# Performance work log

Measured on AMD Instinct MI355X. Metric: run time of the kernel, lower is better.

Reference implementation:

```python
import jax, jax.numpy as jnp
import numpy as np

N_NODES = 100000
N_EDGES = 1600000
HIDDEN = 64
IN_DIM = 3
OUT_DIM = 2
N_MP = 3


def setup_inputs() -> dict:
    key = jax.random.key(0)
    ks = jax.random.split(key, 16)
    x = jax.random.normal(ks[0], (N_NODES, IN_DIM), dtype=jnp.float32)
    edge_index = jax.random.randint(ks[1], (2, N_EDGES), 0, N_NODES, dtype=jnp.int64)

    def lin(k, fan_in, fan_out):
        s = 1.0 / np.sqrt(fan_in)
        return jax.random.uniform(k, (fan_out, fan_in), jnp.float32, -s, s)

    inp = {
        'x': x,
        'edge_index': edge_index,
        'preW': lin(ks[2], IN_DIM, HIDDEN),
        'preb': jnp.zeros((HIDDEN,), jnp.float32),
        'postW': lin(ks[3], HIDDEN, OUT_DIM),
        'postb': jnp.zeros((OUT_DIM,), jnp.float32),
    }
    for i in range(N_MP):
        inp[f'relW{i}'] = lin(ks[4 + 3 * i], HIDDEN, HIDDEN)
        inp[f'relb{i}'] = jnp.zeros((HIDDEN,), jnp.float32)
        inp[f'rootW{i}'] = lin(ks[5 + 3 * i], HIDDEN, HIDDEN)
    return inp


def _graph_conv(h, src, dst, relW, relb, rootW):
    # PyG GraphConv: out_i = W_rel @ (sum_{j in N(i)} h_j) + b_rel + W_root @ h_i
    agg = jax.ops.segment_sum(h[src], dst, num_segments=N_NODES)  # [N, H] scatter-add
    return agg @ relW.T + relb + h @ rootW.T


def reference(x, edge_index, preW, preb, postW, postb,
              relW0, relb0, rootW0, relW1, relb1, rootW1, relW2, relb2, rootW2):
    src, dst = edge_index[0], edge_index[1]
    # pre-MP dense
    h = jax.nn.relu(x @ preW.T + preb)
    # message passing layers (GraphConv, aggr='add'), relu after each
    for relW, relb, rootW in ((relW0, relb0, rootW0),
                              (relW1, relb1, rootW1),
                              (relW2, relb2, rootW2)):
        h = jax.nn.relu(_graph_conv(h, src, dst, relW, relb, rootW))
    # post-MP dense (activation applied to final layer too, as in source)
    out = jax.nn.relu(h @ postW.T + postb)
    return out
```

## Files before the change

### kernel.cpp

```cpp
#include <hip/hip_runtime.h>
#include <hip/hip_fp16.h>

#define N_NODES 100000
#define N_EDGES 1600000
#define HID 64

#define BSH 8
#define NBKT ((N_NODES + 255) / 256)
#define CAP 6144
#define TILE 4096
#define NCHUNK ((N_EDGES + TILE - 1) / TILE)

#define HSC 0.015625f
#define HSCI 64.0f

typedef _Float16 f16x8 __attribute__((ext_vector_type(8)));
typedef float f32x4 __attribute__((ext_vector_type(4)));

__global__ void __launch_bounds__(512) fused0_kernel(
    const int* __restrict__ src, const int* __restrict__ dst,
    int* __restrict__ bcur, unsigned int* __restrict__ tmp,
    const float* __restrict__ x, const float* __restrict__ preW,
    const float* __restrict__ preb, const float* __restrict__ relW,
    const float* __restrict__ relb, const float* __restrict__ rootW,
    __half* __restrict__ m, __half* __restrict__ aout) {
    extern __shared__ __align__(16) char smem[];
    int tid = threadIdx.x;
    if (blockIdx.x < NCHUNK) {
        unsigned long long* ed = (unsigned long long*)smem;
        int* cnt = (int*)(smem + 32768);
        int* cnt2 = (int*)(smem + 34368);
        int* scnx = (int*)(smem + 35968);
        int* gbase = (int*)(smem + 37568);
        int* s = (int*)(smem + 39168);
        int bstart = blockIdx.x * TILE;
        int tcnt = N_EDGES - bstart;
        if (tcnt > TILE) tcnt = TILE;
        if (tcnt < 0) tcnt = 0;
        for (int b = tid; b < NBKT; b += 512) { cnt[b] = 0; cnt2[b] = 0; }
        __syncthreads();
        for (int i = tid; i < tcnt; i += 512) atomicAdd(&cnt[dst[bstart + i] >> BSH], 1);
        __syncthreads();
        s[tid] = (tid < NBKT) ? cnt[tid] : 0;
        __syncthreads();
        for (int off = 1; off < 512; off <<= 1) {
            int add = (tid >= off) ? s[tid - off] : 0;
            __syncthreads();
            s[tid] += add;
            __syncthreads();
        }
        if (tid < NBKT) {
            scnx[tid] = s[tid] - cnt[tid];
            gbase[tid] = tid * CAP + atomicAdd(&bcur[tid], cnt[tid]);
        }
        __syncthreads();
        for (int i = tid; i < tcnt; i += 512) {
            int e = bstart + i;
            int d = dst[e], sc = src[e];
            int b = d >> BSH;
            int pos = scnx[b] + atomicAdd(&cnt2[b], 1);
            ed[pos] = ((unsigned long long)(unsigned)d << 32) | (unsigned)sc;
        }
        __syncthreads();
        for (int i = tid; i < tcnt; i += 512) {
            unsigned long long v = ed[i];
            int d = (int)(v >> 32);
            unsigned sc = (unsigned)v;
            int b = d >> BSH;
            int idx = gbase[b] + (i - scnx[b]);
            if (idx < (b + 1) * CAP)
                tmp[idx] = ((unsigned)(d & 255) << 17) | sc;
        }
    } else {
        __half* hs = (__half*)smem;
        __half* ws = (__half*)(smem + 16384);
        float* xs = (float*)(smem + 32768);
        float* pw = (float*)(smem + 34304);
        float* pbs = (float*)(smem + 35072);
        int g = blockIdx.x - NCHUNK;
        int i0 = g * 128;
#pragma unroll
        for (int it = 0; it < 2; it++) {
            int t = it * 512 + tid;
            int row = t >> 3, c = t & 7;
            const float* wsrc = (row < 64) ? &relW[row * 64 + c * 8]
                                           : &rootW[(row - 64) * 64 + c * 8];
            float4 w0 = *(const float4*)wsrc;
            float4 w1 = *(const float4*)(wsrc + 4);
            uint4 pk;
            __half2* hp = (__half2*)&pk;
            hp[0] = __floats2half2_rn(w0.x, w0.y);
            hp[1] = __floats2half2_rn(w0.z, w0.w);
            hp[2] = __floats2half2_rn(w1.x, w1.y);
            hp[3] = __floats2half2_rn(w1.z, w1.w);
            *(uint4*)&ws[row * 64 + ((c ^ (row & 7)) << 3)] = pk;
        }
        if (tid < 192) pw[tid] = preW[tid];
        if (tid < 64) pbs[tid] = preb[tid];
        if (tid < 384) {
            int gi = i0 * 3 + tid;
            xs[tid] = (gi < N_NODES * 3) ? x[gi] : 0.f;
        }
        __syncthreads();
#pragma unroll
        for (int it = 0; it < 2; it++) {
            int t = it * 512 + tid;
            int row = t >> 3, c = t & 7;
            float v[8];
#pragma unroll
            for (int u = 0; u < 8; u++) {
                int col = c * 8 + u;
                float sv = pbs[col];
                sv = fmaf(xs[row * 3 + 0], pw[col * 3 + 0], sv);
                sv = fmaf(xs[row * 3 + 1], pw[col * 3 + 1], sv);
                sv = fmaf(xs[row * 3 + 2], pw[col * 3 + 2], sv);
                v[u] = fmaxf(sv, 0.f);
            }
            uint4 pk;
            __half2* hp = (__half2*)&pk;
            hp[0] = __floats2half2_rn(v[0], v[1]);
            hp[1] = __floats2half2_rn(v[2], v[3]);
            hp[2] = __floats2half2_rn(v[4], v[5]);
            hp[3] = __floats2half2_rn(v[6], v[7]);
            *(uint4*)&hs[row * 64 + ((c ^ (row & 7)) << 3)] = pk;
        }
        __syncthreads();
        int lane = tid & 63;
        int w = tid >> 6;
        int wm = w >> 1, wn = w & 1;
        int r = lane & 15, q = lane >> 4;
        f32x4 acc[2][4];
#pragma unroll
        for (int mt = 0; mt < 2; mt++)
#pragma unroll
            for (int nt = 0; nt < 4; nt++) acc[mt][nt] = (f32x4){0.f, 0.f, 0.f, 0.f};
#pragma unroll
        for (int ks = 0; ks < 2; ks++) {
            f16x8 af[2], bf[4];
#pragma unroll
            for (int mt = 0; mt < 2; mt++) {
                int row = wm * 32 + mt * 16 + r;
                int cc = (ks * 4 + q) ^ (row & 7);
                af[mt] = *(const f16x8*)&hs[row * 64 + (cc << 3)];
            }
#pragma unroll
            for (int nt = 0; nt < 4; nt++) {
                int row = wn * 64 + nt * 16 + r;
                int cc = (ks * 4 + q) ^ (row & 7);
                bf[nt] = *(const f16x8*)&ws[row * 64 + (cc << 3)];
            }
#pragma unroll
            for (int mt = 0; mt < 2; mt++)
#pragma unroll
                for (int nt = 0; nt < 4; nt++)
                    acc[mt][nt] = __builtin_amdgcn_mfma_f32_16x16x32_f16(af[mt], bf[nt],
                                                                         acc[mt][nt], 0, 0, 0);
        }
        if (wn == 0) {
#pragma unroll
            for (int mt = 0; mt < 2; mt++) {
                int nb = i0 + wm * 32 + mt * 16 + q * 4;
#pragma unroll
                for (int reg = 0; reg < 4; reg++) {
                    int node = nb + reg;
                    if (node >= N_NODES) continue;
#pragma unroll
                    for (int nt = 0; nt < 4; nt++)
                        m[(long)node * 64 + nt * 16 + r] = __float2half(acc[mt][nt][reg]);
                }
            }
        } else {
            float rb[4];
#pragma unroll
            for (int nt = 0; nt < 4; nt++) rb[nt] = relb[nt * 16 + r] * HSC;
#pragma unroll
            for (int mt = 0; mt < 2; mt++) {
                int nb = i0 + wm * 32 + mt * 16 + q * 4;
#pragma unroll
                for (int reg = 0; reg < 4; reg++) {
                    int node = nb + reg;
                    if (node >= N_NODES) continue;
#pragma unroll
                    for (int nt = 0; nt < 4; nt++)
                        aout[(long)node * 64 + nt * 16 + r] =
                            __float2half(fmaf(acc[mt][nt][reg], HSC, rb[nt]));
                }
            }
        }
    }
}

__global__ void __launch_bounds__(256) passb_kernel(const unsigned int* __restrict__ tmp,
                                                    const int* __restrict__ bcur,
                                                    int* __restrict__ rowp,
                                                    int* __restrict__ ssrc) {
    __shared__ int red[256];
    __shared__ int cnt[256], s[256], cur[256];
    int tid = threadIdx.x;
    int b = blockIdx.x;
    int acc = 0;
    for (int i = tid; i < b; i += 256) {
        int c = bcur[i];
        if (c > CAP) c = CAP;
        acc += c;
    }
    red[tid] = acc;
    __syncthreads();
    for (int off = 128; off >= 1; off >>= 1) {
        if (tid < off) red[tid] += red[tid + off];
        __syncthreads();
    }
    int lo = red[0];
    int ne = bcur[b];
    if (ne > CAP) ne = CAP;
    if (b == NBKT - 1 && tid == 0) rowp[N_NODES] = lo + ne;
    int lo_t = b * CAP;
    cnt[tid] = 0;
    __syncthreads();
    for (int i = tid; i < ne; i += 256) atomicAdd(&cnt[tmp[lo_t + i] >> 17], 1);
    __syncthreads();
    int v = cnt[tid];
    s[tid] = v;
    __syncthreads();
    for (int off = 1; off < 256; off <<= 1) {
        int a = (tid >= off) ? s[tid - off] : 0;
        __syncthreads();
        s[tid] += a;
        __syncthreads();
    }
    int excl = lo + s[tid] - v;
    int node = (b << BSH) + tid;
    if (node < N_NODES) rowp[node] = excl;
    cur[tid] = excl;
    __syncthreads();
    for (int i = tid; i < ne; i += 256) {
        unsigned u = tmp[lo_t + i];
        int pos = atomicAdd(&cur[u >> 17], 1);
        ssrc[pos] = (int)(u & 0x1FFFF);
    }
}

__global__ void __launch_bounds__(256) gemmt_kernel(const __half* __restrict__ h,
                                                    const float* __restrict__ relW,
                                                    const float* __restrict__ relb,
                                                    const float* __restrict__ rootW,
                                                    __half* __restrict__ m,
                                                    __half* __restrict__ aout) {
    __shared__ __align__(16) __half hs[128 * 64];
    __shared__ __align__(16) __half ws[128 * 64];
    int tid = threadIdx.x;
    int i0 = blockIdx.x * 128;
#pragma unroll
    for (int it = 0; it < 4; it++) {
        int t = it * 256 + tid;
        int row = t >> 3, c = t & 7;
        const float* wsrc = (row < 64) ? &relW[row * 64 + c * 8]
                                       : &rootW[(row - 64) * 64 + c * 8];
        float4 w0 = *(const float4*)wsrc;
        float4 w1 = *(const float4*)(wsrc + 4);
        uint4 pk;
        __half2* hp = (__half2*)&pk;
        hp[0] = __floats2half2_rn(w0.x, w0.y);
        hp[1] = __floats2half2_rn(w0.z, w0.w);
        hp[2] = __floats2half2_rn(w1.x, w1.y);
        hp[3] = __floats2half2_rn(w1.z, w1.w);
        *(uint4*)&ws[row * 64 + ((c ^ (row & 7)) << 3)] = pk;
    }
#pragma unroll
    for (int it = 0; it < 4; it++) {
        int t = it * 256 + tid;
        int row = t >> 3, c = t & 7;
        uint4 hv = {0u, 0u, 0u, 0u};
        if (i0 + row < N_NODES) hv = *(const uint4*)(h + (long)(i0 + row) * 64 + c * 8);
        *(uint4*)&hs[row * 64 + ((c ^ (row & 7)) << 3)] = hv;
    }
    __syncthreads();

    int lane = tid & 63;
    int w = tid >> 6;
    int wm = w >> 1, wn = w & 1;
    int r = lane & 15, q = lane >> 4;
    f32x4 acc[4][4];
#pragma unroll
    for (int mt = 0; mt < 4; mt++)
#pragma unroll
        for (int nt = 0; nt < 4; nt++) acc[mt][nt] = (f32x4){0.f, 0.f, 0.f, 0.f};
#pragma unroll
    for (int ks = 0; ks < 2; ks++) {
        f16x8 af[4], bf[4];
#pragma unroll
        for (int mt = 0; mt < 4; mt++) {
            int row = wm * 64 + mt * 16 + r;
            int cc = (ks * 4 + q) ^ (row & 7);
            af[mt] = *(const f16x8*)&hs[row * 64 + (cc << 3)];
        }
#pragma unroll
        for (int nt = 0; nt < 4; nt++) {
            int row = wn * 64 + nt * 16 + r;
            int cc = (ks * 4 + q) ^ (row & 7);
            bf[nt] = *(const f16x8*)&ws[row * 64 + (cc << 3)];
        }
#pragma unroll
        for (int mt = 0; mt < 4; mt++)
#pragma unroll
            for (int nt = 0; nt < 4; nt++)
                acc[mt][nt] = __builtin_amdgcn_mfma_f32_16x16x32_f16(af[mt], bf[nt],
                                                                     acc[mt][nt], 0, 0, 0);
    }
    if (wn == 0) {
#pragma unroll
        for (int mt = 0; mt < 4; mt++) {
            int nb = i0 + wm * 64 + mt * 16 + q * 4;
#pragma unroll
            for (int reg = 0; reg < 4; reg++) {
                int node = nb + reg;
                if (node >= N_NODES) continue;
#pragma unroll
                for (int nt = 0; nt < 4; nt++)
                    m[(long)node * 64 + nt * 16 + r] = __float2half(acc[mt][nt][reg]);
            }
        }
    } else {
        float rb[4];
#pragma unroll
        for (int nt = 0; nt < 4; nt++) rb[nt] = relb[nt * 16 + r] * HSC;
#pragma unroll
        for (int mt = 0; mt < 4; mt++) {
            int nb = i0 + wm * 64 + mt * 16 + q * 4;
#pragma unroll
            for (int reg = 0; reg < 4; reg++) {
                int node = nb + reg;
                if (node >= N_NODES) continue;
#pragma unroll
                for (int nt = 0; nt < 4; nt++)
                    aout[(long)node * 64 + nt * 16 + r] =
                        __float2half(fmaf(acc[mt][nt][reg], 1.0f, rb[nt]));
            }
        }
    }
}

template <int FINAL>
__global__ void gather_kernel(const __half* __restrict__ m, __half* __restrict__ a,
                              const int* __restrict__ rowp, const int* __restrict__ ssrc,
                              float aggscale,
                              const float* __restrict__ postW, const float* __restrict__ postb,
                              float* __restrict__ out) {
    int lane = threadIdx.x & 63;
    int wv = (blockIdx.x * blockDim.x + threadIdx.x) >> 6;
    int pb = wv * 4;
    if (pb >= N_NODES) return;
    int n = lane >> 4;
    int g = (lane >> 3) & 1;
    int f8 = (lane & 7) << 3;
    pb = __builtin_amdgcn_readfirstlane(pb);
    int q0 = rowp[pb], q1 = rowp[pb + 1], q2 = rowp[pb + 2];
    int q3 = rowp[pb + 3], q4 = rowp[pb + 4];
    int node = pb + n;
    int r0 = (n == 0) ? q0 : (n == 1) ? q1 : (n == 2) ? q2 : q3;
    int r1 = (n == 0) ? q1 : (n == 1) ? q2 : (n == 2) ? q3 : q4;
    int nedge = r1 - r0;
    uint4 av = *(const uint4*)(a + (long)node * 64 + f8);
    float a0 = 0.f, a1 = 0.f, a2 = 0.f, a3 = 0.f, a4 = 0.f, a5 = 0.f, a6 = 0.f, a7 = 0.f;
#define ACC8(u)                                                         \
    {                                                                   \
        float2 f_;                                                      \
        f_ = __half22float2(*(__half2*)&(u).x); a0 += f_.x; a1 += f_.y; \
        f_ = __half22float2(*(__half2*)&(u).y); a2 += f_.x; a3 += f_.y; \
        f_ = __half22float2(*(__half2*)&(u).z); a4 += f_.x; a5 += f_.y; \
        f_ = __half22float2(*(__half2*)&(u).w); a6 += f_.x; a7 += f_.y; \
    }
    int ns = nedge >> 1;
    int q = 0;
    for (; q + 4 <= ns; q += 4) {
        int b0 = r0 + q * 2 + g;
        int i0 = ssrc[b0];
        int i1 = ssrc[b0 + 2];
        int i2 = ssrc[b0 + 4];
        int i3 = ssrc[b0 + 6];
        uint4 u0 = *(const uint4*)(m + (long)i0 * 64 + f8);
        uint4 u1 = *(const uint4*)(m + (long)i1 * 64 + f8);
        uint4 u2 = *(const uint4*)(m + (long)i2 * 64 + f8);
        uint4 u3 = *(const uint4*)(m + (long)i3 * 64 + f8);
        ACC8(u0); ACC8(u1); ACC8(u2); ACC8(u3);
    }
    if (q + 2 <= ns) {
        int b0 = r0 + q * 2 + g;
        int i0 = ssrc[b0];
        int i1 = ssrc[b0 + 2];
        uint4 u0 = *(const uint4*)(m + (long)i0 * 64 + f8);
        uint4 u1 = *(const uint4*)(m + (long)i1 * 64 + f8);
        ACC8(u0); ACC8(u1);
        q += 2;
    }
    if (q < ns) {
        int i0 = ssrc[r0 + q * 2 + g];
        uint4 u0 = *(const uint4*)(m + (long)i0 * 64 + f8);
        ACC8(u0);
    }
    if ((nedge & 1) && g == 0) {
        int i0 = ssrc[r0 + ns * 2];
        uint4 u0 = *(const uint4*)(m + (long)i0 * 64 + f8);
        ACC8(u0);
    }
#undef ACC8
    a0 += __shfl_xor(a0, 8, 64); a1 += __shfl_xor(a1, 8, 64);
    a2 += __shfl_xor(a2, 8, 64); a3 += __shfl_xor(a3, 8, 64);
    a4 += __shfl_xor(a4, 8, 64); a5 += __shfl_xor(a5, 8, 64);
    a6 += __shfl_xor(a6, 8, 64); a7 += __shfl_xor(a7, 8, 64);
    a0 *= aggscale; a1 *= aggscale; a2 *= aggscale; a3 *= aggscale;
    a4 *= aggscale; a5 *= aggscale; a6 *= aggscale; a7 *= aggscale;
    const __half2* ap = (const __half2*)&av;
    float2 o0 = __half22float2(ap[0]), o1 = __half22float2(ap[1]);
    float2 o2 = __half22float2(ap[2]), o3 = __half22float2(ap[3]);
    a0 = fmaxf(fmaf(o0.x, HSCI, a0), 0.f); a1 = fmaxf(fmaf(o0.y, HSCI, a1), 0.f);
    a2 = fmaxf(fmaf(o1.x, HSCI, a2), 0.f); a3 = fmaxf(fmaf(o1.y, HSCI, a3), 0.f);
    a4 = fmaxf(fmaf(o2.x, HSCI, a4), 0.f); a5 = fmaxf(fmaf(o2.y, HSCI, a5), 0.f);
    a6 = fmaxf(fmaf(o3.x, HSCI, a6), 0.f); a7 = fmaxf(fmaf(o3.y, HSCI, a7), 0.f);
    if (FINAL) {
        float4 w0 = *(const float4*)(postW + f8);
        float4 w1 = *(const float4*)(postW + f8 + 4);
        float4 w2 = *(const float4*)(postW + 64 + f8);
        float4 w3 = *(const float4*)(postW + 64 + f8 + 4);
        float p0 = a0 * w0.x + a1 * w0.y + a2 * w0.z + a3 * w0.w +
                   a4 * w1.x + a5 * w1.y + a6 * w1.z + a7 * w1.w;
        float p1 = a0 * w2.x + a1 * w2.y + a2 * w2.z + a3 * w2.w +
                   a4 * w3.x + a5 * w3.y + a6 * w3.z + a7 * w3.w;
#pragma unroll
        for (int off = 1; off <= 4; off <<= 1) {
            p0 += __shfl_xor(p0, off, 64);
            p1 += __shfl_xor(p1, off, 64);
        }
        if ((lane & 15) == 0) {
            out[(long)node * 2 + 0] = fmaxf(p0 + postb[0], 0.f);
            out[(long)node * 2 + 1] = fmaxf(p1 + postb[1], 0.f);
        }
    } else {
        if (g == 0) {
            uint4 st;
            __half2* sp = (__half2*)&st;
            sp[0] = __floats2half2_rn(a0 * HSC, a1 * HSC);
            sp[1] = __floats2half2_rn(a2 * HSC, a3 * HSC);
            sp[2] = __floats2half2_rn(a4 * HSC, a5 * HSC);
            sp[3] = __floats2half2_rn(a6 * HSC, a7 * HSC);
            *(uint4*)(a + (long)node * 64 + f8) = st;
        }
    }
}

extern "C" void kernel_launch(void* const* d_in, const int* in_sizes, int n_in,
                              void* d_out, int out_size, void* d_ws, size_t ws_size,
                              hipStream_t stream) {
    const float* x = (const float*)d_in[0];
    const int* esrc = (const int*)d_in[1];
    const int* edst = esrc + N_EDGES;
    const float* preW = (const float*)d_in[2];
    const float* preb = (const float*)d_in[3];
    const float* postW = (const float*)d_in[4];
    const float* postb = (const float*)d_in[5];
    const float* relW[3] = {(const float*)d_in[6], (const float*)d_in[9], (const float*)d_in[12]};
    const float* relb[3] = {(const float*)d_in[7], (const float*)d_in[10], (const float*)d_in[13]};
    const float* rootW[3] = {(const float*)d_in[8], (const float*)d_in[11], (const float*)d_in[14]};
    float* out = (float*)d_out;

    const size_t NF = (size_t)N_NODES * HID;
    char* p = (char*)d_ws;
    __half* hA = (__half*)p; p += NF * 2;
    __half* hB = (__half*)p; p += NF * 2;
    __half* mB = (__half*)p; p += NF * 2;
    p = (char*)(((size_t)p + 255) & ~(size_t)255);
    int* rowp = (int*)p; p += (size_t)(N_NODES + 1) * 4;
    p = (char*)(((size_t)p + 255) & ~(size_t)255);
    int* ssrc = (int*)p; p += (size_t)N_EDGES * 4;
    p = (char*)(((size_t)p + 255) & ~(size_t)255);
    unsigned int* tmp = (unsigned int*)p; p += (size_t)NBKT * CAP * 4;
    int* bcur = (int*)p; p += 512 * 4;

    const int GEMM_BLOCKS = (N_NODES + 127) / 128;
    const int GATHER_BLOCKS = N_NODES / 16;
    const float IS1 = 64.0f;

    hipMemsetAsync(bcur, 0, 512 * 4, stream);
    fused0_kernel<<<NCHUNK + GEMM_BLOCKS, 512, 41216, stream>>>(
        esrc, edst, bcur, tmp, x, preW, preb, relW[0], relb[0], rootW[0], mB, hB);
    passb_kernel<<<NBKT, 256, 0, stream>>>(tmp, bcur, rowp, ssrc);

    gather_kernel<0><<<GATHER_BLOCKS, 256, 0, stream>>>(mB, hB, rowp, ssrc, 1.0f,
                                                        nullptr, nullptr, nullptr);
    gemmt_kernel<<<GEMM_BLOCKS, 256, 0, stream>>>(hB, relW[1], relb[1], rootW[1], mB, hA);
    gather_kernel<0><<<GATHER_BLOCKS, 256, 0, stream>>>(mB, hA, rowp, ssrc, IS1,
                                                        nullptr, nullptr, nullptr);
    gemmt_kernel<<<GEMM_BLOCKS, 256, 0, stream>>>(hA, relW[2], relb[2], rootW[2], mB, hB);
    gather_kernel<1><<<GATHER_BLOCKS, 256, 0, stream>>>(mB, hB, rowp, ssrc, IS1,
                                                        postW, postb, out);
}
```

Measured before the change: 252.2 us.

## Fuse neighbor gather-aggregate into the following GEMM kernel via shared memory

Merges the gather (segment-sum plus root term and ReLU) for layers 1 and 2 with the next layer's rel/root GEMM. The aggregated node features go straight into shared memory as the MFMA A operand instead of a half-precision intermediate in global memory. This removes two kernel launches and one write and read of the N×64 hidden tensor per fused layer, using ping-pong m/a buffers. The cost is 512-thread blocks where each block does both irregular gather work and the GEMM, so load imbalance from edge degrees now stalls the MFMA phase.

```diff
diff --git a/kernel.cpp b/kernel.cpp
--- a/kernel.cpp
+++ b/kernel.cpp
@@ -240,19 +240,22 @@
     }
 }
 
-__global__ void __launch_bounds__(256) gemmt_kernel(const __half* __restrict__ h,
-                                                    const float* __restrict__ relW,
-                                                    const float* __restrict__ relb,
-                                                    const float* __restrict__ rootW,
-                                                    __half* __restrict__ m,
-                                                    __half* __restrict__ aout) {
+__global__ void __launch_bounds__(512) gg_kernel(
+    const __half* __restrict__ m_in, const __half* __restrict__ aout_in,
+    const int* __restrict__ rowp, const int* __restrict__ ssrc,
+    float aggscale,
+    const float* __restrict__ relW, const float* __restrict__ relb,
+    const float* __restrict__ rootW,
+    __half* __restrict__ m_out, __half* __restrict__ aout_out) {
     __shared__ __align__(16) __half hs[128 * 64];
     __shared__ __align__(16) __half ws[128 * 64];
     int tid = threadIdx.x;
     int i0 = blockIdx.x * 128;
-#pragma unroll
-    for (int it = 0; it < 4; it++) {
-        int t = it * 256 + tid;
+    int lane = tid & 63;
+    int w = tid >> 6;
+#pragma unroll
+    for (int it = 0; it < 2; it++) {
+        int t = it * 512 + tid;
         int row = t >> 3, c = t & 7;
         const float* wsrc = (row < 64) ? &relW[row * 64 + c * 8]
                                        : &rootW[(row - 64) * 64 + c * 8];
@@ -266,31 +269,108 @@
         hp[3] = __floats2half2_rn(w1.z, w1.w);
         *(uint4*)&ws[row * 64 + ((c ^ (row & 7)) << 3)] = pk;
     }
-#pragma unroll
-    for (int it = 0; it < 4; it++) {
-        int t = it * 256 + tid;
-        int row = t >> 3, c = t & 7;
-        uint4 hv = {0u, 0u, 0u, 0u};
-        if (i0 + row < N_NODES) hv = *(const uint4*)(h + (long)(i0 + row) * 64 + c * 8);
-        *(uint4*)&hs[row * 64 + ((c ^ (row & 7)) << 3)] = hv;
+    int n = lane >> 4;
+    int g = (lane >> 3) & 1;
+    int f8 = (lane & 7) << 3;
+#pragma unroll
+    for (int pass = 0; pass < 4; pass++) {
+        int nl = pass * 32 + (w << 2);
+        int pb = __builtin_amdgcn_readfirstlane(i0 + nl);
+        int x0 = pb + 0 < N_NODES ? pb + 0 : N_NODES;
+        int x1 = pb + 1 < N_NODES ? pb + 1 : N_NODES;
+        int x2 = pb + 2 < N_NODES ? pb + 2 : N_NODES;
+        int x3 = pb + 3 < N_NODES ? pb + 3 : N_NODES;
+        int x4 = pb + 4 < N_NODES ? pb + 4 : N_NODES;
+        int q0 = rowp[x0], q1 = rowp[x1], q2 = rowp[x2], q3 = rowp[x3], q4 = rowp[x4];
+        int node = pb + n;
+        int r0 = (n == 0) ? q0 : (n == 1) ? q1 : (n == 2) ? q2 : q3;
+        int r1 = (n == 0) ? q1 : (n == 1) ? q2 : (n == 2) ? q3 : q4;
+        int nedge = r1 - r0;
+        uint4 av = {0u, 0u, 0u, 0u};
+        if (node < N_NODES) av = *(const uint4*)(aout_in + (long)node * 64 + f8);
+        float a0 = 0.f, a1 = 0.f, a2 = 0.f, a3 = 0.f;
+        float a4 = 0.f, a5 = 0.f, a6 = 0.f, a7 = 0.f;
+#define ACC8(u)                                                         \
+    {                                                                   \
+        float2 f_;                                                      \
+        f_ = __half22float2(*(__half2*)&(u).x); a0 += f_.x; a1 += f_.y; \
+        f_ = __half22float2(*(__half2*)&(u).y); a2 += f_.x; a3 += f_.y; \
+        f_ = __half22float2(*(__half2*)&(u).z); a4 += f_.x; a5 += f_.y; \
+        f_ = __half22float2(*(__half2*)&(u).w); a6 += f_.x; a7 += f_.y; \
+    }
+        int ns = nedge >> 1;
+        int qq = 0;
+        for (; qq + 4 <= ns; qq += 4) {
+            int b0 = r0 + qq * 2 + g;
+            int i0e = ssrc[b0];
+            int i1e = ssrc[b0 + 2];
+            int i2e = ssrc[b0 + 4];
+            int i3e = ssrc[b0 + 6];
+            uint4 u0 = *(const uint4*)(m_in + (long)i0e * 64 + f8);
+            uint4 u1 = *(const uint4*)(m_in + (long)i1e * 64 + f8);
+            uint4 u2 = *(const uint4*)(m_in + (long)i2e * 64 + f8);
+            uint4 u3 = *(const uint4*)(m_in + (long)i3e * 64 + f8);
+            ACC8(u0); ACC8(u1); ACC8(u2); ACC8(u3);
+        }
+        if (qq + 2 <= ns) {
+            int b0 = r0 + qq * 2 + g;
+            int i0e = ssrc[b0];
+            int i1e = ssrc[b0 + 2];
+            uint4 u0 = *(const uint4*)(m_in + (long)i0e * 64 + f8);
+            uint4 u1 = *(const uint4*)(m_in + (long)i1e * 64 + f8);
+            ACC8(u0); ACC8(u1);
+            qq += 2;
+        }
+        if (qq < ns) {
+            int i0e = ssrc[r0 + qq * 2 + g];
+            uint4 u0 = *(const uint4*)(m_in + (long)i0e * 64 + f8);
+            ACC8(u0);
+        }
+        if ((nedge & 1) && g == 0) {
+            int i0e = ssrc[r0 + ns * 2];
+            uint4 u0 = *(const uint4*)(m_in + (long)i0e * 64 + f8);
+            ACC8(u0);
+        }
+#undef ACC8
+        a0 += __shfl_xor(a0, 8, 64); a1 += __shfl_xor(a1, 8, 64);
+        a2 += __shfl_xor(a2, 8, 64); a3 += __shfl_xor(a3, 8, 64);
+        a4 += __shfl_xor(a4, 8, 64); a5 += __shfl_xor(a5, 8, 64);
+        a6 += __shfl_xor(a6, 8, 64); a7 += __shfl_xor(a7, 8, 64);
+        a0 *= aggscale; a1 *= aggscale; a2 *= aggscale; a3 *= aggscale;
+        a4 *= aggscale; a5 *= aggscale; a6 *= aggscale; a7 *= aggscale;
+        const __half2* ap = (const __half2*)&av;
+        float2 o0 = __half22float2(ap[0]), o1 = __half22float2(ap[1]);
+        float2 o2 = __half22float2(ap[2]), o3 = __half22float2(ap[3]);
+        a0 = fmaxf(fmaf(o0.x, HSCI, a0), 0.f); a1 = fmaxf(fmaf(o0.y, HSCI, a1), 0.f);
+        a2 = fmaxf(fmaf(o1.x, HSCI, a2), 0.f); a3 = fmaxf(fmaf(o1.y, HSCI, a3), 0.f);
+        a4 = fmaxf(fmaf(o2.x, HSCI, a4), 0.f); a5 = fmaxf(fmaf(o2.y, HSCI, a5), 0.f);
+        a6 = fmaxf(fmaf(o3.x, HSCI, a6), 0.f); a7 = fmaxf(fmaf(o3.y, HSCI, a7), 0.f);
+        if (g == 0) {
+            int row = nl + n;
+            int c = lane & 7;
+            uint4 st;
+            __half2* sp = (__half2*)&st;
+            sp[0] = __floats2half2_rn(a0 * HSC, a1 * HSC);
+            sp[1] = __floats2half2_rn(a2 * HSC, a3 * HSC);
+            sp[2] = __floats2half2_rn(a4 * HSC, a5 * HSC);
+            sp[3] = __floats2half2_rn(a6 * HSC, a7 * HSC);
+            *(uint4*)&hs[row * 64 + ((c ^ (row & 7)) << 3)] = st;
+        }
     }
     __syncthreads();
-
-    int lane = tid & 63;
-    int w = tid >> 6;
     int wm = w >> 1, wn = w & 1;
     int r = lane & 15, q = lane >> 4;
-    f32x4 acc[4][4];
-#pragma unroll
-    for (int mt = 0; mt < 4; mt++)
+    f32x4 acc[2][4];
+#pragma unroll
+    for (int mt = 0; mt < 2; mt++)
 #pragma unroll
         for (int nt = 0; nt < 4; nt++) acc[mt][nt] = (f32x4){0.f, 0.f, 0.f, 0.f};
 #pragma unroll
     for (int ks = 0; ks < 2; ks++) {
-        f16x8 af[4], bf[4];
-#pragma unroll
-        for (int mt = 0; mt < 4; mt++) {
-            int row = wm * 64 + mt * 16 + r;
+        f16x8 af[2], bf[4];
+#pragma unroll
+        for (int mt = 0; mt < 2; mt++) {
+            int row = wm * 32 + mt * 16 + r;
             int cc = (ks * 4 + q) ^ (row & 7);
             af[mt] = *(const f16x8*)&hs[row * 64 + (cc << 3)];
         }
@@ -301,7 +381,7 @@
             bf[nt] = *(const f16x8*)&ws[row * 64 + (cc << 3)];
         }
 #pragma unroll
-        for (int mt = 0; mt < 4; mt++)
+        for (int mt = 0; mt < 2; mt++)
 #pragma unroll
             for (int nt = 0; nt < 4; nt++)
                 acc[mt][nt] = __builtin_amdgcn_mfma_f32_16x16x32_f16(af[mt], bf[nt],
@@ -309,15 +389,15 @@
     }
     if (wn == 0) {
 #pragma unroll
-        for (int mt = 0; mt < 4; mt++) {
-            int nb = i0 + wm * 64 + mt * 16 + q * 4;
+        for (int mt = 0; mt < 2; mt++) {
+            int nb = i0 + wm * 32 + mt * 16 + q * 4;
 #pragma unroll
             for (int reg = 0; reg < 4; reg++) {
                 int node = nb + reg;
                 if (node >= N_NODES) continue;
 #pragma unroll
                 for (int nt = 0; nt < 4; nt++)
-                    m[(long)node * 64 + nt * 16 + r] = __float2half(acc[mt][nt][reg]);
+                    m_out[(long)node * 64 + nt * 16 + r] = __float2half(acc[mt][nt][reg]);
             }
         }
     } else {
@@ -325,16 +405,16 @@
 #pragma unroll
         for (int nt = 0; nt < 4; nt++) rb[nt] = relb[nt * 16 + r] * HSC;
 #pragma unroll
-        for (int mt = 0; mt < 4; mt++) {
-            int nb = i0 + wm * 64 + mt * 16 + q * 4;
+        for (int mt = 0; mt < 2; mt++) {
+            int nb = i0 + wm * 32 + mt * 16 + q * 4;
 #pragma unroll
             for (int reg = 0; reg < 4; reg++) {
                 int node = nb + reg;
                 if (node >= N_NODES) continue;
 #pragma unroll
                 for (int nt = 0; nt < 4; nt++)
-                    aout[(long)node * 64 + nt * 16 + r] =
-                        __float2half(fmaf(acc[mt][nt][reg], 1.0f, rb[nt]));
+                    aout_out[(long)node * 64 + nt * 16 + r] =
+                        __float2half(acc[mt][nt][reg] + rb[nt]);
             }
         }
     }
@@ -465,9 +545,10 @@
 
     const size_t NF = (size_t)N_NODES * HID;
     char* p = (char*)d_ws;
-    __half* hA = (__half*)p; p += NF * 2;
-    __half* hB = (__half*)p; p += NF * 2;
+    __half* mA = (__half*)p; p += NF * 2;
     __half* mB = (__half*)p; p += NF * 2;
+    __half* aA = (__half*)p; p += NF * 2;
+    __half* aB = (__half*)p; p += NF * 2;
     p = (char*)(((size_t)p + 255) & ~(size_t)255);
     int* rowp = (int*)p; p += (size_t)(N_NODES + 1) * 4;
     p = (char*)(((size_t)p + 255) & ~(size_t)255);
@@ -482,15 +563,12 @@
 
     hipMemsetAsync(bcur, 0, 512 * 4, stream);
     fused0_kernel<<<NCHUNK + GEMM_BLOCKS, 512, 41216, stream>>>(
-        esrc, edst, bcur, tmp, x, preW, preb, relW[0], relb[0], rootW[0], mB, hB);
+        esrc, edst, bcur, tmp, x, preW, preb, relW[0], relb[0], rootW[0], mA, aA);
     passb_kernel<<<NBKT, 256, 0, stream>>>(tmp, bcur, rowp, ssrc);
-
-    gather_kernel<0><<<GATHER_BLOCKS, 256, 0, stream>>>(mB, hB, rowp, ssrc, 1.0f,
-                                                        nullptr, nullptr, nullptr);
-    gemmt_kernel<<<GEMM_BLOCKS, 256, 0, stream>>>(hB, relW[1], relb[1], rootW[1], mB, hA);
-    gather_kernel<0><<<GATHER_BLOCKS, 256, 0, stream>>>(mB, hA, rowp, ssrc, IS1,
-                                                        nullptr, nullptr, nullptr);
-    gemmt_kernel<<<GEMM_BLOCKS, 256, 0, stream>>>(hA, relW[2], relb[2], rootW[2], mB, hB);
-    gather_kernel<1><<<GATHER_BLOCKS, 256, 0, stream>>>(mB, hB, rowp, ssrc, IS1,
+    gg_kernel<<<GEMM_BLOCKS, 512, 0, stream>>>(mA, aA, rowp, ssrc, 1.0f,
+                                               relW[1], relb[1], rootW[1], mB, aB);
+    gg_kernel<<<GEMM_BLOCKS, 512, 0, stream>>>(mB, aB, rowp, ssrc, IS1,
+                                               relW[2], relb[2], rootW[2], mA, aA);
+    gather_kernel<1><<<GATHER_BLOCKS, 256, 0, stream>>>(mA, aA, rowp, ssrc, IS1,
                                                         postW, postb, out);
 }
```

Result: no change. 254.0 us (+0.7%).
